# Kernel tuning notes

Measured on AMD Instinct MI355X. Metric: run time of the kernel, lower is better.

Reference implementation:

```python
import jax, jax.numpy as jnp
import numpy as np

NUM_FIELDS = 40
EMBED_DIM = 64
IN_SUB = 40
OUT_SUB = 40
BATCH = 256


def setup_inputs() -> dict:
    key = jax.random.key(0)
    k0, k1 = jax.random.split(key)
    B0 = jax.random.normal(k0, (BATCH, NUM_FIELDS, EMBED_DIM), dtype=jnp.float32)
    Bi = jax.random.normal(k1, (BATCH, IN_SUB, EMBED_DIM), dtype=jnp.float32)
    # parameters, initialized exactly as in the torch module
    W = jnp.tile(jnp.eye(EMBED_DIM, dtype=jnp.float32)[None], (OUT_SUB, 1, 1))  # (n, D, D)
    alpha = jnp.ones((NUM_FIELDS, IN_SUB, OUT_SUB), dtype=jnp.float32)          # (f, i, n)
    h = jnp.ones((OUT_SUB, EMBED_DIM, 1), dtype=jnp.float32)                    # (n, D, 1)
    return {"B0": B0, "Bi": Bi, "W": W, "alpha": alpha, "h": h}


def reference(B0, Bi, W, alpha, h):
    # Math of the original: fusion[b,n,D,d] = sum_{f,i} B0[b,f,D]*Bi[b,i,d]*alpha[f,i,n]
    # (equivalent to the 5D outer product contracted with alpha, but never
    #  materializes the (b,f,i,D,D) tensor).
    fusion = jnp.einsum('bfD,bid,fin->bnDd', B0, Bi, alpha)  # (b, n, D, D)
    # elementwise scale by W then project with h: out[b,n,D] = sum_d fusion*W*h
    out = jnp.einsum('bnDd,nDd,nd->bnD', fusion, W, h[..., 0])
    return out
```

## Files before the change

kernel.cpp:

```cpp
#include <hip/hip_runtime.h>
#include <hip/hip_bf16.h>

#define NF 40
#define NI 40
#define NN 40
#define ED 64
#define NB 256

typedef __attribute__((ext_vector_type(8))) short   short8;
typedef __attribute__((ext_vector_type(8))) __bf16  bf16x8;
typedef __attribute__((ext_vector_type(4))) float   f32x4;

__device__ __forceinline__ unsigned short f2bf(float x) {
    union { float f; unsigned u; } v; v.f = x;
    unsigned r = v.u + 0x7FFFu + ((v.u >> 16) & 1u);
    return (unsigned short)(r >> 16);
}

__device__ __forceinline__ bf16x8 ld_frag(const unsigned short* p) {
    return __builtin_bit_cast(bf16x8, *(const short8*)p);
}

__device__ __forceinline__ f32x4 mfma16(bf16x8 a, bf16x8 b, f32x4 c) {
    return __builtin_amdgcn_mfma_f32_16x16x32_bf16(a, b, c, 0, 0, 0);
}

#define WHP_N (64 * 64)
#define ALP_N (48 * 64)

__global__ __launch_bounds__(256) void gif_prep4(
        const float* __restrict__ W, const float* __restrict__ alpha,
        const float* __restrict__ h,
        unsigned short* __restrict__ whp, unsigned short* __restrict__ alp) {
    const int x = blockIdx.x;
    const int t = threadIdx.x;
    if (x < NN) {
        const int n = x;
        for (int idx = t; idx < 64 * 64; idx += 256) {
            int d = idx & 63;
            whp[n * WHP_N + idx] = f2bf(W[n * ED * ED + idx] * h[n * ED + d]);
        }
        for (int idx = t; idx < 8 * 64; idx += 256)
            alp[n * ALP_N + (40 + (idx >> 6)) * 64 + (idx & 63)] = 0;
        for (int idx = t; idx < 40 * 24; idx += 256) {
            int i = idx / 24, f = 40 + idx - i * 24;
            alp[n * ALP_N + i * 64 + f] = 0;
        }
    } else {
        const int f = x - NN;
        for (int idx = t; idx < NI * NN; idx += 256) {
            int i = idx / NN, n = idx - i * NN;
            alp[n * ALP_N + i * 64 + f] = f2bf(alpha[(f * NI + i) * NN + n]);
        }
    }
}

#define PSM 72
__global__ __launch_bounds__(256, 2) void gif_main8(
        const float* __restrict__ B0, const float* __restrict__ Bi,
        const unsigned short* __restrict__ whp,
        const unsigned short* __restrict__ alp,
        float* __restrict__ out) {
    const int bg = blockIdx.x;
    const int ng = blockIdx.y;
    const int t = threadIdx.x;
    const int lane = t & 63, w = t >> 6;
    const int quad = lane >> 4, l15 = lane & 15, fo = quad * 8;
    const int n = ng * 4 + w;

    __shared__ __align__(16) unsigned short sBi[48 * PSM];
    __shared__ __align__(16) unsigned short sBT[64 * PSM];

    float4 rbi[3], rb0[3];
    {
        const float4* biv = (const float4*)(Bi + (size_t)(bg * 4) * NI * ED);
        const float4* b0v = (const float4*)(B0 + (size_t)(bg * 4) * NF * ED);
#pragma unroll
        for (int k = 0; k < 3; ++k) {
            const int c = t + k * 256;
            if (c < 640) { rbi[k] = biv[c]; rb0[k] = b0v[c]; }
        }
    }

    bf16x8 alA[3][2], whB[4][2];
    {
        const unsigned short* ap = alp + n * ALP_N;
        const unsigned short* wp = whp + n * WHP_N;
#pragma unroll
        for (int m = 0; m < 3; ++m)
#pragma unroll
            for (int s = 0; s < 2; ++s)
                alA[m][s] = ld_frag(&ap[(m * 16 + l15) * 64 + s * 32 + fo]);
#pragma unroll
        for (int tt = 0; tt < 4; ++tt)
#pragma unroll
            for (int s = 0; s < 2; ++s)
                whB[tt][s] = ld_frag(&wp[(tt * 16 + l15) * 64 + s * 32 + fo]);
    }

    for (int idx = t; idx < 8 * 64; idx += 256)
        sBi[(40 + (idx >> 6)) * PSM + (idx & 63)] = 0;
    for (int idx = t; idx < 64 * 24; idx += 256) {
        int D = idx / 24, f = 40 + idx - D * 24;
        sBT[D * PSM + f] = 0;
    }

#pragma unroll
    for (int k = 0; k < 3; ++k) {
        const int c = t + k * 256;
        if (c < 640) {
            const int r = c >> 4, col = (c & 15) * 4;
            ushort4 pk;
            pk.x = f2bf(rbi[k].x); pk.y = f2bf(rbi[k].y);
            pk.z = f2bf(rbi[k].z); pk.w = f2bf(rbi[k].w);
            *(ushort4*)&sBi[r * PSM + col] = pk;
            sBT[(col + 0) * PSM + r] = f2bf(rb0[k].x);
            sBT[(col + 1) * PSM + r] = f2bf(rb0[k].y);
            sBT[(col + 2) * PSM + r] = f2bf(rb0[k].z);
            sBT[(col + 3) * PSM + r] = f2bf(rb0[k].w);
        }
    }
    __syncthreads();

#pragma unroll
    for (int j = 0; j < 4; ++j) {
        const int b = bg * 4 + j;

        if (j < 3) {
            const float4* biv = (const float4*)(Bi + (size_t)(b + 1) * NI * ED);
            const float4* b0v = (const float4*)(B0 + (size_t)(b + 1) * NF * ED);
#pragma unroll
            for (int k = 0; k < 3; ++k) {
                const int c = t + k * 256;
                if (c < 640) { rbi[k] = biv[c]; rb0[k] = b0v[c]; }
            }
        }

        bf16x8 biA[3][2];
#pragma unroll
        for (int m = 0; m < 3; ++m)
#pragma unroll
            for (int s = 0; s < 2; ++s)
                biA[m][s] = ld_frag(&sBi[(m * 16 + l15) * PSM + s * 32 + fo]);

        float p[4];
#pragma unroll
        for (int tt = 0; tt < 4; ++tt) {
            bf16x8 bb0 = ld_frag(&sBT[(tt * 16 + l15) * PSM + fo]);
            bf16x8 bb1 = ld_frag(&sBT[(tt * 16 + l15) * PSM + 32 + fo]);
            float acc = 0.f;
#pragma unroll
            for (int m = 0; m < 3; ++m) {
                f32x4 z = {0.f, 0.f, 0.f, 0.f};
                f32x4 T = mfma16(biA[m][0], whB[tt][0], z);
                T = mfma16(biA[m][1], whB[tt][1], T);
                f32x4 G = mfma16(alA[m][0], bb0, z);
                G = mfma16(alA[m][1], bb1, G);
                acc += T[0] * G[0] + T[1] * G[1] + T[2] * G[2] + T[3] * G[3];
            }
            p[tt] = acc;
        }
#pragma unroll
        for (int tt = 0; tt < 4; ++tt) {
            p[tt] += __shfl_xor(p[tt], 16, 64);
            p[tt] += __shfl_xor(p[tt], 32, 64);
        }
        float v = (quad == 0) ? p[0] : (quad == 1) ? p[1] : (quad == 2) ? p[2] : p[3];
        out[((size_t)b * NN + n) * ED + lane] = v;

        if (j < 3) {
            __syncthreads();
#pragma unroll
            for (int k = 0; k < 3; ++k) {
                const int c = t + k * 256;
                if (c < 640) {
                    const int r = c >> 4, col = (c & 15) * 4;
                    ushort4 pk;
                    pk.x = f2bf(rbi[k].x); pk.y = f2bf(rbi[k].y);
                    pk.z = f2bf(rbi[k].z); pk.w = f2bf(rbi[k].w);
                    *(ushort4*)&sBi[r * PSM + col] = pk;
                    sBT[(col + 0) * PSM + r] = f2bf(rb0[k].x);
                    sBT[(col + 1) * PSM + r] = f2bf(rb0[k].y);
                    sBT[(col + 2) * PSM + r] = f2bf(rb0[k].z);
                    sBT[(col + 3) * PSM + r] = f2bf(rb0[k].w);
                }
            }
            __syncthreads();
        }
    }
}

#define PS 72
#define WH_N (ED * PS)
#define AL_N (48 * PS)

__global__ __launch_bounds__(256) void gif_prep(
        const float* __restrict__ W, const float* __restrict__ alpha,
        const float* __restrict__ h,
        unsigned short* __restrict__ whp, unsigned short* __restrict__ alp) {
    const int n = blockIdx.x;
    const int t0 = blockIdx.y * 256 + threadIdx.x;
    for (int idx = t0; idx < ED * PS; idx += 1024) {
        int D = idx / PS, c = idx - D * PS;
        float v = (c < ED) ? W[n * ED * ED + D * ED + c] * h[n * ED + c] : 0.f;
        whp[n * WH_N + idx] = f2bf(v);
    }
    for (int idx = t0; idx < 48 * PS; idx += 1024) {
        int i = idx / PS, c = idx - i * PS;
        float v = (i < NI && c < NF) ? alpha[(c * NI + i) * NN + n] : 0.f;
        alp[n * AL_N + idx] = f2bf(v);
    }
}

__device__ __forceinline__ bf16x8 mk_al_frag(const float* __restrict__ alpha,
        int n, int m, int s, int l15, int quad) {
    bf16x8 r;
    const int row = m * 16 + l15;
    const int f0 = s * 32 + quad * 8;
#pragma unroll
    for (int j = 0; j < 8; ++j) {
        const int f = f0 + j;
        float v = (row < NI && f < NF) ? alpha[(f * NI + row) * NN + n] : 0.f;
        r[j] = (__bf16)v;
    }
    return r;
}
__device__ __forceinline__ bf16x8 mk_wh_frag(const float* __restrict__ W,
        const float* __restrict__ h, int n, int tt, int s, int l15, int quad) {
    bf16x8 r;
    const int row = tt * 16 + l15;
    const int k0 = s * 32 + quad * 8;
#pragma unroll
    for (int j = 0; j < 8; ++j) {
        float v = W[n * ED * ED + row * ED + k0 + j] * h[n * ED + k0 + j];
        r[j] = (__bf16)v;
    }
    return r;
}

__global__ __launch_bounds__(256) void gif_mfma(
        const float* __restrict__ B0, const float* __restrict__ Bi,
        const unsigned short* __restrict__ whp, const unsigned short* __restrict__ alp,
        const float* __restrict__ W, const float* __restrict__ alpha,
        const float* __restrict__ h, int useWs, float* __restrict__ out) {
    const int q = blockIdx.x >> 8;
    const int b = blockIdx.x & 255;

    __shared__ __align__(16) unsigned short sBi[48 * PS];
    __shared__ __align__(16) unsigned short sBT[ED * PS];

    const int t = threadIdx.x;
    for (int idx = t; idx < 48 * PS; idx += 256) {
        int i = idx / PS, c = idx - i * PS;
        sBi[idx] = (i < NI && c < ED) ? f2bf(Bi[b * NI * ED + i * ED + c])
                                      : (unsigned short)0;
    }
    for (int idx = t; idx < ED * PS; idx += 256) {
        int D = idx / PS, c = idx - D * PS;
        sBT[idx] = (c < NF) ? f2bf(B0[b * NF * ED + c * ED + D])
                            : (unsigned short)0;
    }
    __syncthreads();

    const int lane = t & 63, w = t >> 6;
    const int quad = lane >> 4, l15 = lane & 15;
    const int fragoff = quad * 8;

    bf16x8 biA[3][2], b0B[4][2];
#pragma unroll
    for (int m = 0; m < 3; ++m)
#pragma unroll
        for (int s = 0; s < 2; ++s)
            biA[m][s] = ld_frag(&sBi[(m * 16 + l15) * PS + s * 32 + fragoff]);
#pragma unroll
    for (int tt = 0; tt < 4; ++tt)
#pragma unroll
        for (int s = 0; s < 2; ++s)
            b0B[tt][s] = ld_frag(&sBT[(tt * 16 + l15) * PS + s * 32 + fragoff]);

#pragma unroll
    for (int rep = 0; rep < 2; ++rep) {
        const int n = q * 8 + w + rep * 4;

        bf16x8 alA[3][2];
        if (useWs) {
#pragma unroll
            for (int m = 0; m < 3; ++m)
#pragma unroll
                for (int s = 0; s < 2; ++s)
                    alA[m][s] = ld_frag(&alp[n * AL_N + (m * 16 + l15) * PS + s * 32 + fragoff]);
        } else {
#pragma unroll
            for (int m = 0; m < 3; ++m)
#pragma unroll
                for (int s = 0; s < 2; ++s)
                    alA[m][s] = mk_al_frag(alpha, n, m, s, l15, quad);
        }

        float p[4];
#pragma unroll
        for (int tt = 0; tt < 4; ++tt) {
            bf16x8 whB2[2];
            if (useWs) {
                const unsigned short* wpp = &whp[n * WH_N + (tt * 16 + l15) * PS + fragoff];
                whB2[0] = ld_frag(wpp);
                whB2[1] = ld_frag(wpp + 32);
            } else {
                whB2[0] = mk_wh_frag(W, h, n, tt, 0, l15, quad);
                whB2[1] = mk_wh_frag(W, h, n, tt, 1, l15, quad);
            }
            float acc = 0.f;
#pragma unroll
            for (int m = 0; m < 3; ++m) {
                f32x4 z = {0.f, 0.f, 0.f, 0.f};
                f32x4 T = mfma16(biA[m][0], whB2[0], z);
                T = mfma16(biA[m][1], whB2[1], T);
                f32x4 G = mfma16(alA[m][0], b0B[tt][0], z);
                G = mfma16(alA[m][1], b0B[tt][1], G);
                acc += T[0] * G[0] + T[1] * G[1] + T[2] * G[2] + T[3] * G[3];
            }
            p[tt] = acc;
        }
#pragma unroll
        for (int tt = 0; tt < 4; ++tt) {
            p[tt] += __shfl_xor(p[tt], 16, 64);
            p[tt] += __shfl_xor(p[tt], 32, 64);
        }
        float v = (quad == 0) ? p[0] : (quad == 1) ? p[1] : (quad == 2) ? p[2] : p[3];
        out[(b * NN + n) * ED + lane] = v;
    }
}

extern "C" void kernel_launch(void* const* d_in, const int* in_sizes, int n_in,
                              void* d_out, int out_size, void* d_ws, size_t ws_size,
                              hipStream_t stream) {
    const float* B0    = (const float*)d_in[0];
    const float* Bi    = (const float*)d_in[1];
    const float* W     = (const float*)d_in[2];
    const float* alpha = (const float*)d_in[3];
    const float* h     = (const float*)d_in[4];
    float* out = (float*)d_out;

    const size_t need2 = (size_t)(NN * WHP_N + NN * ALP_N) * sizeof(unsigned short);
    if (ws_size >= need2) {
        unsigned short* whp = (unsigned short*)d_ws;
        unsigned short* alp = whp + (size_t)NN * WHP_N;
        gif_prep4<<<NN + NF, 256, 0, stream>>>(W, alpha, h, whp, alp);
        gif_main8<<<dim3(64, 10), 256, 0, stream>>>(B0, Bi, whp, alp, out);
        return;
    }

    const size_t need1 = (size_t)(NN * WH_N + NN * AL_N) * sizeof(unsigned short);
    const int useWs = (ws_size >= need1) ? 1 : 0;
    unsigned short* whp = (unsigned short*)d_ws;
    unsigned short* alp = whp + (size_t)NN * WH_N;
    if (useWs) {
        gif_prep<<<dim3(NN, 4), 256, 0, stream>>>(W, alpha, h, whp, alp);
    }
    gif_mfma<<<5 * NB, 256, 0, stream>>>(B0, Bi, whp, alp, W, alpha, h, useWs, out);
}
```

Baseline: 81.53 us.

## Pre-convert B0/Bi to padded bf16 workspace and stream per-batch tiles in main kernel

A prep kernel now converts Bi to bf16 padded rows and B0 to a transposed, padded bf16 layout in workspace, alongside the weight/alpha prep. A new main kernel then loads these pre-laid-out tiles with 16-byte vector loads into registers, prefetching the next batch while computing the current one, and keeps alpha and W*h fragments in registers across four batches. This is meant to remove the in-kernel fp32 conversion and the scattered transposed LDS writes from the hot loop. In exchange it adds an extra global round trip for the activations and needs a larger workspace, falling back to the old path otherwise.

Result: slower. 93.85 us (+15.1%).

```diff
diff --git a/kernel.cpp b/kernel.cpp
--- a/kernel.cpp
+++ b/kernel.cpp
@@ -25,8 +25,178 @@
     return __builtin_amdgcn_mfma_f32_16x16x32_bf16(a, b, c, 0, 0, 0);
 }
 
+#define BIP_N (48 * 64)
+#define B0T_N (64 * 64)
 #define WHP_N (64 * 64)
 #define ALP_N (48 * 64)
+
+__global__ __launch_bounds__(256) void gif_prep6(
+        const float* __restrict__ B0, const float* __restrict__ Bi,
+        const float* __restrict__ W, const float* __restrict__ alpha,
+        const float* __restrict__ h,
+        unsigned short* __restrict__ BiP, unsigned short* __restrict__ B0T,
+        unsigned short* __restrict__ whp, unsigned short* __restrict__ alp) {
+    const int x = blockIdx.x;
+    const int t = threadIdx.x;
+
+    if (x < NB) {
+        const int b = x;
+        __shared__ float sB0[NF][ED + 1];
+        for (int idx = t; idx < NF * ED; idx += 256) {
+            int f = idx >> 6, D = idx & 63;
+            sB0[f][D] = B0[b * NF * ED + idx];
+        }
+        __syncthreads();
+        for (int idx = t; idx < 48 * 64; idx += 256) {
+            int i = idx >> 6, d = idx & 63;
+            BiP[b * BIP_N + idx] = (i < NI) ? f2bf(Bi[b * NI * ED + i * ED + d])
+                                            : (unsigned short)0;
+        }
+        for (int idx = t; idx < 64 * 64; idx += 256) {
+            int D = idx >> 6, f = idx & 63;
+            B0T[b * B0T_N + idx] = (f < NF) ? f2bf(sB0[f][D]) : (unsigned short)0;
+        }
+    } else if (x < NB + NN) {
+        const int n = x - NB;
+        for (int idx = t; idx < 64 * 64; idx += 256) {
+            int d = idx & 63;
+            whp[n * WHP_N + idx] = f2bf(W[n * ED * ED + idx] * h[n * ED + d]);
+        }
+        for (int idx = t; idx < 8 * 64; idx += 256)
+            alp[n * ALP_N + (40 + (idx >> 6)) * 64 + (idx & 63)] = 0;
+        for (int idx = t; idx < 40 * 24; idx += 256) {
+            int i = idx / 24, f = 40 + idx - i * 24;
+            alp[n * ALP_N + i * 64 + f] = 0;
+        }
+    } else {
+        const int f = x - NB - NN;
+        for (int idx = t; idx < NI * NN; idx += 256) {
+            int i = idx / NN, n = idx - i * NN;
+            alp[n * ALP_N + i * 64 + f] = f2bf(alpha[(f * NI + i) * NN + n]);
+        }
+    }
+}
+
+#define PSM 72
+#define NCH 896
+
+__global__ __launch_bounds__(256, 2) void gif_main9(
+        const unsigned short* __restrict__ BiP,
+        const unsigned short* __restrict__ B0T,
+        const unsigned short* __restrict__ whp,
+        const unsigned short* __restrict__ alp,
+        float* __restrict__ out) {
+    const int bg = blockIdx.x;
+    const int ng = blockIdx.y;
+    const int t = threadIdx.x;
+    const int lane = t & 63, w = t >> 6;
+    const int quad = lane >> 4, l15 = lane & 15, fo = quad * 8;
+    const int n = ng * 4 + w;
+
+    __shared__ __align__(16) unsigned short sBi[48 * PSM];
+    __shared__ __align__(16) unsigned short sBT[64 * PSM];
+
+    int4 creg[4];
+    {
+        const int4* bip = (const int4*)(BiP + (size_t)(bg * 4) * BIP_N);
+        const int4* b0t = (const int4*)(B0T + (size_t)(bg * 4) * B0T_N);
+#pragma unroll
+        for (int k = 0; k < 4; ++k) {
+            const int c = t + k * 256;
+            if (c < NCH) creg[k] = (c < 384) ? bip[c] : b0t[c - 384];
+        }
+    }
+
+    bf16x8 alA[3][2], whB[4][2];
+    {
+        const unsigned short* ap = alp + n * ALP_N;
+        const unsigned short* wp = whp + n * WHP_N;
+#pragma unroll
+        for (int m = 0; m < 3; ++m)
+#pragma unroll
+            for (int s = 0; s < 2; ++s)
+                alA[m][s] = ld_frag(&ap[(m * 16 + l15) * 64 + s * 32 + fo]);
+#pragma unroll
+        for (int tt = 0; tt < 4; ++tt)
+#pragma unroll
+            for (int s = 0; s < 2; ++s)
+                whB[tt][s] = ld_frag(&wp[(tt * 16 + l15) * 64 + s * 32 + fo]);
+    }
+
+#pragma unroll
+    for (int k = 0; k < 4; ++k) {
+        const int c = t + k * 256;
+        if (c < NCH) {
+            unsigned short* dst = (c < 384)
+                ? &sBi[(c >> 3) * PSM + (c & 7) * 8]
+                : &sBT[((c - 384) >> 3) * PSM + ((c - 384) & 7) * 8];
+            *(int4*)dst = creg[k];
+        }
+    }
+    __syncthreads();
+
+#pragma unroll
+    for (int j = 0; j < 4; ++j) {
+        const int b = bg * 4 + j;
+
+        if (j < 3) {
+            const int4* bip = (const int4*)(BiP + (size_t)(b + 1) * BIP_N);
+            const int4* b0t = (const int4*)(B0T + (size_t)(b + 1) * B0T_N);
+#pragma unroll
+            for (int k = 0; k < 4; ++k) {
+                const int c = t + k * 256;
+                if (c < NCH) creg[k] = (c < 384) ? bip[c] : b0t[c - 384];
+            }
+        }
+
+        bf16x8 biA[3][2];
+#pragma unroll
+        for (int m = 0; m < 3; ++m)
+#pragma unroll
+            for (int s = 0; s < 2; ++s)
+                biA[m][s] = ld_frag(&sBi[(m * 16 + l15) * PSM + s * 32 + fo]);
+
+        float p[4];
+#pragma unroll
+        for (int tt = 0; tt < 4; ++tt) {
+            bf16x8 bb0 = ld_frag(&sBT[(tt * 16 + l15) * PSM + fo]);
+            bf16x8 bb1 = ld_frag(&sBT[(tt * 16 + l15) * PSM + 32 + fo]);
+            float acc = 0.f;
+#pragma unroll
+            for (int m = 0; m < 3; ++m) {
+                f32x4 z = {0.f, 0.f, 0.f, 0.f};
+                f32x4 T = mfma16(biA[m][0], whB[tt][0], z);
+                T = mfma16(biA[m][1], whB[tt][1], T);
+                f32x4 G = mfma16(alA[m][0], bb0, z);
+                G = mfma16(alA[m][1], bb1, G);
+                acc += T[0] * G[0] + T[1] * G[1] + T[2] * G[2] + T[3] * G[3];
+            }
+            p[tt] = acc;
+        }
+#pragma unroll
+        for (int tt = 0; tt < 4; ++tt) {
+            p[tt] += __shfl_xor(p[tt], 16, 64);
+            p[tt] += __shfl_xor(p[tt], 32, 64);
+        }
+        float v = (quad == 0) ? p[0] : (quad == 1) ? p[1] : (quad == 2) ? p[2] : p[3];
+        out[((size_t)b * NN + n) * ED + lane] = v;
+
+        if (j < 3) {
+            __syncthreads();
+#pragma unroll
+            for (int k = 0; k < 4; ++k) {
+                const int c = t + k * 256;
+                if (c < NCH) {
+                    unsigned short* dst = (c < 384)
+                        ? &sBi[(c >> 3) * PSM + (c & 7) * 8]
+                        : &sBT[((c - 384) >> 3) * PSM + ((c - 384) & 7) * 8];
+                    *(int4*)dst = creg[k];
+                }
+            }
+            __syncthreads();
+        }
+    }
+}
 
 __global__ __launch_bounds__(256) void gif_prep4(
         const float* __restrict__ W, const float* __restrict__ alpha,
@@ -55,7 +225,6 @@
     }
 }
 
-#define PSM 72
 __global__ __launch_bounds__(256, 2) void gif_main8(
         const float* __restrict__ B0, const float* __restrict__ Bi,
         const unsigned short* __restrict__ whp,
@@ -194,24 +363,6 @@
 #define WH_N (ED * PS)
 #define AL_N (48 * PS)
 
-__global__ __launch_bounds__(256) void gif_prep(
-        const float* __restrict__ W, const float* __restrict__ alpha,
-        const float* __restrict__ h,
-        unsigned short* __restrict__ whp, unsigned short* __restrict__ alp) {
-    const int n = blockIdx.x;
-    const int t0 = blockIdx.y * 256 + threadIdx.x;
-    for (int idx = t0; idx < ED * PS; idx += 1024) {
-        int D = idx / PS, c = idx - D * PS;
-        float v = (c < ED) ? W[n * ED * ED + D * ED + c] * h[n * ED + c] : 0.f;
-        whp[n * WH_N + idx] = f2bf(v);
-    }
-    for (int idx = t0; idx < 48 * PS; idx += 1024) {
-        int i = idx / PS, c = idx - i * PS;
-        float v = (i < NI && c < NF) ? alpha[(c * NI + i) * NN + n] : 0.f;
-        alp[n * AL_N + idx] = f2bf(v);
-    }
-}
-
 __device__ __forceinline__ bf16x8 mk_al_frag(const float* __restrict__ alpha,
         int n, int m, int s, int l15, int quad) {
     bf16x8 r;
@@ -240,9 +391,8 @@
 
 __global__ __launch_bounds__(256) void gif_mfma(
         const float* __restrict__ B0, const float* __restrict__ Bi,
-        const unsigned short* __restrict__ whp, const unsigned short* __restrict__ alp,
         const float* __restrict__ W, const float* __restrict__ alpha,
-        const float* __restrict__ h, int useWs, float* __restrict__ out) {
+        const float* __restrict__ h, float* __restrict__ out) {
     const int q = blockIdx.x >> 8;
     const int b = blockIdx.x & 255;
 
@@ -283,32 +433,18 @@
         const int n = q * 8 + w + rep * 4;
 
         bf16x8 alA[3][2];
-        if (useWs) {
-#pragma unroll
-            for (int m = 0; m < 3; ++m)
-#pragma unroll
-                for (int s = 0; s < 2; ++s)
-                    alA[m][s] = ld_frag(&alp[n * AL_N + (m * 16 + l15) * PS + s * 32 + fragoff]);
-        } else {
-#pragma unroll
-            for (int m = 0; m < 3; ++m)
-#pragma unroll
-                for (int s = 0; s < 2; ++s)
-                    alA[m][s] = mk_al_frag(alpha, n, m, s, l15, quad);
-        }
+#pragma unroll
+        for (int m = 0; m < 3; ++m)
+#pragma unroll
+            for (int s = 0; s < 2; ++s)
+                alA[m][s] = mk_al_frag(alpha, n, m, s, l15, quad);
 
         float p[4];
 #pragma unroll
         for (int tt = 0; tt < 4; ++tt) {
             bf16x8 whB2[2];
-            if (useWs) {
-                const unsigned short* wpp = &whp[n * WH_N + (tt * 16 + l15) * PS + fragoff];
-                whB2[0] = ld_frag(wpp);
-                whB2[1] = ld_frag(wpp + 32);
-            } else {
-                whB2[0] = mk_wh_frag(W, h, n, tt, 0, l15, quad);
-                whB2[1] = mk_wh_frag(W, h, n, tt, 1, l15, quad);
-            }
+            whB2[0] = mk_wh_frag(W, h, n, tt, 0, l15, quad);
+            whB2[1] = mk_wh_frag(W, h, n, tt, 1, l15, quad);
             float acc = 0.f;
 #pragma unroll
             for (int m = 0; m < 3; ++m) {
@@ -341,8 +477,20 @@
     const float* h     = (const float*)d_in[4];
     float* out = (float*)d_out;
 
-    const size_t need2 = (size_t)(NN * WHP_N + NN * ALP_N) * sizeof(unsigned short);
+    const size_t need2 =
+        (size_t)(NB * BIP_N + NB * B0T_N + NN * WHP_N + NN * ALP_N) * sizeof(unsigned short);
     if (ws_size >= need2) {
+        unsigned short* BiP = (unsigned short*)d_ws;
+        unsigned short* B0T = BiP + (size_t)NB * BIP_N;
+        unsigned short* whp = B0T + (size_t)NB * B0T_N;
+        unsigned short* alp = whp + (size_t)NN * WHP_N;
+        gif_prep6<<<NB + NN + NF, 256, 0, stream>>>(B0, Bi, W, alpha, h, BiP, B0T, whp, alp);
+        gif_main9<<<dim3(64, 10), 256, 0, stream>>>(BiP, B0T, whp, alp, out);
+        return;
+    }
+
+    const size_t need1 = (size_t)(NN * WHP_N + NN * ALP_N) * sizeof(unsigned short);
+    if (ws_size >= need1) {
         unsigned short* whp = (unsigned short*)d_ws;
         unsigned short* alp = whp + (size_t)NN * WHP_N;
         gif_prep4<<<NN + NF, 256, 0, stream>>>(W, alpha, h, whp, alp);
@@ -350,12 +498,5 @@
         return;
     }
 
-    const size_t need1 = (size_t)(NN * WH_N + NN * AL_N) * sizeof(unsigned short);
-    const int useWs = (ws_size >= need1) ? 1 : 0;
-    unsigned short* whp = (unsigned short*)d_ws;
-    unsigned short* alp = whp + (size_t)NN * WH_N;
-    if (useWs) {
-        gif_prep<<<dim3(NN, 4), 256, 0, stream>>>(W, alpha, h, whp, alp);
-    }
-    gif_mfma<<<5 * NB, 256, 0, stream>>>(B0, Bi, whp, alp, W, alpha, h, useWs, out);
-}
+    gif_mfma<<<5 * NB, 256, 0, stream>>>(B0, Bi, W, alpha, h, out);
+}
```
